# Optimization experiments

Measured on AMD Instinct MI355X. Metric: run time of the kernel, lower is better.

The kernel has to match this reference:

```python
import jax, jax.numpy as jnp
import numpy as np

# Standard icosahedron face list (20 faces over 12 vertices).
ICO_FACES = np.array([
    [0, 11, 5], [0, 5, 1], [0, 1, 7], [0, 7, 10], [0, 10, 11],
    [1, 5, 9], [5, 11, 4], [11, 10, 2], [10, 7, 6], [7, 1, 8],
    [3, 9, 4], [3, 4, 2], [3, 2, 6], [3, 6, 8], [3, 8, 9],
    [4, 9, 5], [2, 4, 11], [6, 2, 10], [8, 6, 7], [9, 8, 1],
], dtype=np.int64)


def _ico_face_adjacency():
    # Faces are adjacent iff they share an edge == share exactly 2 vertices.
    adj = np.zeros((20, 20), dtype=np.float32)
    for i in range(20):
        for j in range(i + 1, 20):
            if len(set(ICO_FACES[i]) & set(ICO_FACES[j])) == 2:
                adj[i, j] = adj[j, i] = 1.0
    return jnp.asarray(adj)


def setup_inputs() -> dict:
    key = jax.random.key(0)
    ks = jax.random.split(key, 9)
    B, D = 65536, 512
    def w(k, fan_in, fan_out):
        return jax.random.normal(k, (fan_in, fan_out), jnp.float32) * (1.0 / np.sqrt(fan_in))
    return {
        "z": jax.random.normal(ks[0], (B, D), jnp.float32),
        "W1": w(ks[1], D, 512), "b1": jnp.zeros((512,), jnp.float32),
        "W2": w(ks[2], 512, 256), "b2": jnp.zeros((256,), jnp.float32),
        "W3": w(ks[3], 256, 128), "b3": jnp.zeros((128,), jnp.float32),
        "W4": w(ks[4], 128, 20), "b4": jnp.zeros((20,), jnp.float32),
        "precomputed_adj": _ico_face_adjacency(),  # [20,20], zero diagonal
    }


def reference(z, W1, b1, W2, b2, W3, b3, W4, b4, precomputed_adj):
    # Eval path: dropout = identity, recon_loss = 0.
    h = jax.nn.relu(z @ W1 + b1)
    h = jax.nn.relu(h @ W2 + b2)
    h = jax.nn.relu(h @ W3 + b3)
    face_probs = jax.nn.sigmoid(h @ W4 + b4)          # [B, 20]
    face_mask = (face_probs > 0.5).astype(z.dtype)    # [B, 20]
    # outer(mask, mask) * precomputed adjacency; diagonal of adj is already 0,
    # reproducing the i != j condition of the original triple loop.
    adj_matrix = face_mask[:, :, None] * face_mask[:, None, :] * precomputed_adj  # [B,20,20]
    recon_loss = jnp.asarray(0.0, jnp.float32)
    return (adj_matrix, face_mask, face_probs, recon_loss)
```

## Files before the change

kernel.cpp:

```cpp
#include <hip/hip_runtime.h>
#include <math.h>

#define NT   1024
#define BR   32
#define TAU  1e-3f
#define LIST_CAP 65536

typedef _Float16 half8 __attribute__((ext_vector_type(8)));
typedef float    f32x4 __attribute__((ext_vector_type(4)));

#define SWZ(r) (((r)&7)<<4)

#define PACK_ELS 425984
#define OFF_LIST 16
#define OFF_PH   (16 + LIST_CAP*4)
#define OFF_PL   (OFF_PH + PACK_ELS*2)
#define WS_PACK_NEED (OFF_PL + PACK_ELS*2)
#define WS_F32_NEED  (16 + LIST_CAP*4)

__device__ __forceinline__ int p1(int c){ return ((c&7)<<6)|(c>>3); }
__device__ __forceinline__ int p2(int c){ return ((c&3)<<6)|(c>>2); }
__device__ __forceinline__ int p3(int c){ return ((c&1)<<6)|(c>>1); }

__global__ void pack_w(const float* __restrict__ W1, const float* __restrict__ W2,
                       const float* __restrict__ W3,
                       _Float16* __restrict__ PH, _Float16* __restrict__ PL) {
    int i = blockIdx.x * 256 + threadIdx.x;
    if (i >= PACK_ELS) return;
    const float* W; int N, KS, loc;
    if (i < 262144)            { W = W1; N = 512; KS = 16; loc = i; }
    else if (i < 393216)       { W = W2; N = 256; KS = 16; loc = i - 262144; }
    else                       { W = W3; N = 128; KS = 8;  loc = i - 393216; }
    int j   = loc & 7;
    int l   = (loc >> 3) & 63;
    int rest = loc >> 9;
    int ks  = rest & (KS - 1);
    int nt  = rest >> (KS == 16 ? 4 : 3);
    int k = ks * 32 + (l >> 4) * 8 + j;
    int n = nt * 16 + (l & 15);
    float v = W[k * N + n];
    _Float16 hi = (_Float16)v;
    _Float16 lo = (_Float16)(v - (float)hi);
    PH[i] = hi; PL[i] = lo;
}

template<int K, int N, int NTW, int MREP, bool SPLIT_OUT>
__device__ __forceinline__ void mfma_layer(const char* __restrict__ actIn,
    const _Float16* __restrict__ PH, const _Float16* __restrict__ PL,
    const float* __restrict__ bias,
    char* __restrict__ actOut, float* __restrict__ h3out,
    int nt0, int m0, int l)
{
    constexpr int KS = K / 32;
    const int r  = l & 15;
    const int kg = l >> 4;
    f32x4 acc[MREP][NTW];
#pragma unroll
    for (int t = 0; t < NTW; ++t) {
        float bb = bias[(nt0 + t) * 16 + r];
#pragma unroll
        for (int m = 0; m < MREP; ++m) acc[m][t] = (f32x4){bb, bb, bb, bb};
    }
    constexpr int loIn = BR * K * 2;
    for (int ks = 0; ks < KS; ++ks) {
        half8 ah[MREP], al[MREP];
#pragma unroll
        for (int m = 0; m < MREP; ++m) {
            int row = (m0 + m) * 16 + r;
            int lin = (row * K + kg * 8 + ks * 32) * 2;
            int sw  = lin ^ SWZ(row);
            ah[m] = *(const half8*)(actIn + sw);
            al[m] = *(const half8*)(actIn + sw + loIn);
        }
#pragma unroll
        for (int t = 0; t < NTW; ++t) {
            const size_t base = ((size_t)((nt0 + t) * KS + ks) * 64 + l) * 8;
            half8 bh = *(const half8*)(PH + base);
            half8 bl = *(const half8*)(PL + base);
#pragma unroll
            for (int m = 0; m < MREP; ++m) {
                acc[m][t] = __builtin_amdgcn_mfma_f32_16x16x32_f16(ah[m], bh, acc[m][t], 0, 0, 0);
                acc[m][t] = __builtin_amdgcn_mfma_f32_16x16x32_f16(ah[m], bl, acc[m][t], 0, 0, 0);
                acc[m][t] = __builtin_amdgcn_mfma_f32_16x16x32_f16(al[m], bh, acc[m][t], 0, 0, 0);
            }
        }
    }
    constexpr int loOut = BR * N * 2;
#pragma unroll
    for (int t = 0; t < NTW; ++t) {
        int n = (nt0 + t) * 16 + r;
#pragma unroll
        for (int m = 0; m < MREP; ++m)
#pragma unroll
        for (int b = 0; b < 4; ++b) {
            int rowD = (m0 + m) * 16 + kg * 4 + b;
            float v = acc[m][t][b];
            v = v > 0.f ? v : 0.f;
            if constexpr (SPLIT_OUT) {
                _Float16 hi = (_Float16)v;
                _Float16 lo = (_Float16)(v - (float)hi);
                int lin = (rowD * N + n) * 2;
                int sw  = lin ^ SWZ(rowD);
                *(_Float16*)(actOut + sw)         = hi;
                *(_Float16*)(actOut + sw + loOut) = lo;
            } else {
                h3out[rowD * 132 + n] = v;
            }
        }
    }
}

__global__ __launch_bounds__(NT, 4)
void dec_mfma(const float* __restrict__ z,
              const float* __restrict__ b1, const float* __restrict__ b2,
              const float* __restrict__ b3,
              const float* __restrict__ W4, const float* __restrict__ b4,
              const float* __restrict__ adj,
              const _Float16* __restrict__ PH, const _Float16* __restrict__ PL,
              float* __restrict__ out, int B,
              int* __restrict__ cnt, int* __restrict__ list)
{
    __shared__ __align__(16) char ldsA[65536];
    __shared__ __align__(16) char ldsB[65536];
    __shared__ float logitsS[BR * 20];
    __shared__ float maskS[BR * 20];
    __shared__ float adjS[400];

    const int tid = threadIdx.x;
    const int w   = tid >> 6;
    const int l   = tid & 63;
    const int rowBase = blockIdx.x * BR;

    const int O_MASK  = B * 400;
    const int O_PROBS = O_MASK + B * 20;
    const int O_LOSS  = O_PROBS + B * 20;

    if (tid < 400) adjS[tid] = adj[tid];

    for (int i = tid; i < BR * 512; i += NT) {
        int r = i >> 9, k = i & 511;
        float v = z[(rowBase + r) * 512 + k];
        _Float16 hi = (_Float16)v;
        _Float16 lo = (_Float16)(v - (float)hi);
        int lin = (r * 512 + k) * 2;
        int sw  = lin ^ SWZ(r);
        *(_Float16*)(ldsA + sw)         = hi;
        *(_Float16*)(ldsA + sw + 32768) = lo;
    }
    __syncthreads();

    mfma_layer<512, 512, 2, 2, true >(ldsA, PH,          PL,          b1, ldsB, nullptr, w * 2, 0, l);
    __syncthreads();
    mfma_layer<512, 256, 1, 2, true >(ldsB, PH + 262144, PL + 262144, b2, ldsA, nullptr, w, 0, l);
    __syncthreads();
    mfma_layer<256, 128, 1, 1, false>(ldsA, PH + 393216, PL + 393216, b3, nullptr, (float*)ldsB, w & 7, w >> 3, l);
    __syncthreads();

    const float* h3 = (const float*)ldsB;
    for (int o = tid; o < BR * 20; o += NT) {
        int r = o / 20, c = o - r * 20;
        float acc = b4[c];
        for (int k = 0; k < 128; ++k)
            acc += h3[r * 132 + k] * W4[k * 20 + c];
        logitsS[o] = acc;
    }
    __syncthreads();

    if (tid < BR) {
        float mn = 1e30f;
#pragma unroll
        for (int c = 0; c < 20; ++c)
            mn = fminf(mn, fabsf(logitsS[tid * 20 + c]));
        if (mn < TAU) {
            int idx = atomicAdd(cnt, 1);
            if (idx < LIST_CAP) list[idx] = rowBase + tid;
        }
    }

    for (int o = tid; o < BR * 20; o += NT) {
        double lg = (double)logitsS[o];
        double p  = 1.0 / (1.0 + exp(-lg));
        out[O_PROBS + rowBase * 20 + o] = (float)p;
        float m = lg > 0.0 ? 1.0f : 0.0f;
        out[O_MASK + rowBase * 20 + o] = m;
        maskS[o] = m;
    }
    __syncthreads();

    for (int o = tid; o < BR * 20; o += NT) {
        int r = o / 20, ii = o - r * 20;
        float mri = maskS[r * 20 + ii];
        float* orow = &out[(rowBase + r) * 400 + ii * 20];
#pragma unroll
        for (int b = 0; b < 5; ++b) {
            float4 v;
            v.x = mri * maskS[r * 20 + 4*b+0] * adjS[ii * 20 + 4*b+0];
            v.y = mri * maskS[r * 20 + 4*b+1] * adjS[ii * 20 + 4*b+1];
            v.z = mri * maskS[r * 20 + 4*b+2] * adjS[ii * 20 + 4*b+2];
            v.w = mri * maskS[r * 20 + 4*b+3] * adjS[ii * 20 + 4*b+3];
            *(float4*)&orow[4*b] = v;
        }
    }

    if (blockIdx.x == 0 && tid == 0) out[O_LOSS] = 0.0f;
}

template<typename T, bool FLAG>
__global__ __launch_bounds__(256, 2)
void dec_fused(const float* __restrict__ z,
               const float* __restrict__ W1, const float* __restrict__ b1,
               const float* __restrict__ W2, const float* __restrict__ b2,
               const float* __restrict__ W3, const float* __restrict__ b3,
               const float* __restrict__ W4, const float* __restrict__ b4,
               const float* __restrict__ adj,
               float* __restrict__ out, int B,
               int* __restrict__ cnt, int* __restrict__ list)
{
    constexpr int STR = (sizeof(T) == 4) ? 20 : 17;
    __shared__ T     hT[512 * STR];
    __shared__ T     logitsS[16 * 20];
    __shared__ float maskS[16 * 20];
    __shared__ float adjS[400];

    const int tid = threadIdx.x;
    const int rg  = tid >> 6;
    const int cg  = tid & 63;
    const int r0  = rg * 4;
    const int rowBase = blockIdx.x * 16;

    const int O_MASK  = B * 400;
    const int O_PROBS = O_MASK + B * 20;
    const int O_LOSS  = O_PROBS + B * 20;

    for (int i = tid; i < 400; i += 256) adjS[i] = adj[i];
    for (int i = tid; i < 512 * 16; i += 256) {
        int k = i & 511, r = i >> 9;
        hT[k * STR + r] = (T)z[(rowBase + r) * 512 + k];
    }
    __syncthreads();
    {
        T a[4][8];
#pragma unroll
        for (int ri = 0; ri < 4; ++ri)
#pragma unroll
            for (int ci = 0; ci < 8; ++ci) a[ri][ci] = (T)0;
#pragma unroll 2
        for (int k = 0; k < 512; ++k) {
            T zr[4];
#pragma unroll
            for (int ri = 0; ri < 4; ++ri) zr[ri] = hT[k * STR + r0 + ri];
            const float4* w1p = (const float4*)(W1 + k * 512 + cg * 8);
            float4 w0 = w1p[0], w1v = w1p[1];
            T wv[8] = {(T)w0.x,(T)w0.y,(T)w0.z,(T)w0.w,
                       (T)w1v.x,(T)w1v.y,(T)w1v.z,(T)w1v.w};
#pragma unroll
            for (int ci = 0; ci < 8; ++ci)
#pragma unroll
                for (int ri = 0; ri < 4; ++ri)
                    a[ri][ci] += zr[ri] * wv[ci];
        }
        __syncthreads();
#pragma unroll
        for (int ci = 0; ci < 8; ++ci) {
            int c = cg * 8 + ci;
            T bb = (T)b1[c]; int cp = p1(c);
#pragma unroll
            for (int ri = 0; ri < 4; ++ri) {
                T v = a[ri][ci] + bb;
                hT[cp * STR + r0 + ri] = v > (T)0 ? v : (T)0;
            }
        }
        __syncthreads();
    }
    {
        T a[4][4];
#pragma unroll
        for (int ri = 0; ri < 4; ++ri)
#pragma unroll
            for (int ci = 0; ci < 4; ++ci) a[ri][ci] = (T)0;
#pragma unroll 2
        for (int k = 0; k < 512; ++k) {
            int kp = p1(k);
            T zr[4];
#pragma unroll
            for (int ri = 0; ri < 4; ++ri) zr[ri] = hT[kp * STR + r0 + ri];
            float4 wq = *(const float4*)(W2 + k * 256 + cg * 4);
            T wv[4] = {(T)wq.x,(T)wq.y,(T)wq.z,(T)wq.w};
#pragma unroll
            for (int ci = 0; ci < 4; ++ci)
#pragma unroll
                for (int ri = 0; ri < 4; ++ri)
                    a[ri][ci] += zr[ri] * wv[ci];
        }
        __syncthreads();
#pragma unroll
        for (int ci = 0; ci < 4; ++ci) {
            int c = cg * 4 + ci;
            T bb = (T)b2[c]; int cp = p2(c);
#pragma unroll
            for (int ri = 0; ri < 4; ++ri) {
                T v = a[ri][ci] + bb;
                hT[cp * STR + r0 + ri] = v > (T)0 ? v : (T)0;
            }
        }
        __syncthreads();
    }
    {
        T a[4][2];
#pragma unroll
        for (int ri = 0; ri < 4; ++ri)
#pragma unroll
            for (int ci = 0; ci < 2; ++ci) a[ri][ci] = (T)0;
#pragma unroll 2
        for (int k = 0; k < 256; ++k) {
            int kp = p2(k);
            T zr[4];
#pragma unroll
            for (int ri = 0; ri < 4; ++ri) zr[ri] = hT[kp * STR + r0 + ri];
            float2 wq = *(const float2*)(W3 + k * 128 + cg * 2);
            T wv[2] = {(T)wq.x,(T)wq.y};
#pragma unroll
            for (int ci = 0; ci < 2; ++ci)
#pragma unroll
                for (int ri = 0; ri < 4; ++ri)
                    a[ri][ci] += zr[ri] * wv[ci];
        }
        __syncthreads();
#pragma unroll
        for (int ci = 0; ci < 2; ++ci) {
            int c = cg * 2 + ci;
            T bb = (T)b3[c]; int cp = p3(c);
#pragma unroll
            for (int ri = 0; ri < 4; ++ri) {
                T v = a[ri][ci] + bb;
                hT[cp * STR + r0 + ri] = v > (T)0 ? v : (T)0;
            }
        }
        __syncthreads();
    }
    for (int o = tid; o < 16 * 20; o += 256) {
        int r = o / 20, c = o - r * 20;
        T acc = (T)b4[c];
        for (int k = 0; k < 128; ++k)
            acc += hT[p3(k) * STR + r] * (T)W4[k * 20 + c];
        logitsS[o] = acc;
    }
    __syncthreads();
    if constexpr (FLAG) {
        if (tid < 16) {
            float mn = 1e30f;
#pragma unroll
            for (int c = 0; c < 20; ++c)
                mn = fminf(mn, fabsf((float)logitsS[tid * 20 + c]));
            if (mn < TAU) {
                int idx = atomicAdd(cnt, 1);
                if (idx < LIST_CAP) list[idx] = rowBase + tid;
            }
        }
    }
    for (int o = tid; o < 16 * 20; o += 256) {
        double lg = (double)logitsS[o];
        double p  = 1.0 / (1.0 + exp(-lg));
        out[O_PROBS + rowBase * 20 + o] = (float)p;
        float m = lg > 0.0 ? 1.0f : 0.0f;
        out[O_MASK + rowBase * 20 + o] = m;
        maskS[o] = m;
    }
    __syncthreads();
    for (int o = tid; o < 16 * 20; o += 256) {
        int r = o / 20, ii = o - r * 20;
        float mri = maskS[r * 20 + ii];
        float* orow = &out[(rowBase + r) * 400 + ii * 20];
#pragma unroll
        for (int b = 0; b < 5; ++b) {
            float4 v;
            v.x = mri * maskS[r * 20 + 4*b+0] * adjS[ii * 20 + 4*b+0];
            v.y = mri * maskS[r * 20 + 4*b+1] * adjS[ii * 20 + 4*b+1];
            v.z = mri * maskS[r * 20 + 4*b+2] * adjS[ii * 20 + 4*b+2];
            v.w = mri * maskS[r * 20 + 4*b+3] * adjS[ii * 20 + 4*b+3];
            *(float4*)&orow[4*b] = v;
        }
    }
    if (blockIdx.x == 0 && tid == 0) out[O_LOSS] = 0.0f;
}

__global__ __launch_bounds__(256, 4)
void repair_rows(const float* __restrict__ z,
                 const float* __restrict__ W1, const float* __restrict__ b1,
                 const float* __restrict__ W2, const float* __restrict__ b2,
                 const float* __restrict__ W3, const float* __restrict__ b3,
                 const float* __restrict__ W4, const float* __restrict__ b4,
                 const float* __restrict__ adj,
                 float* __restrict__ out, int B,
                 const int* __restrict__ cnt, const int* __restrict__ list)
{
    __shared__ double bufA[512];
    __shared__ double bufB[512];
    __shared__ double lgS[20];
    __shared__ float  mskS[20];

    const int tid = threadIdx.x;
    const int O_MASK  = B * 400;
    const int O_PROBS = O_MASK + B * 20;

    int n = *cnt;
    if (n > LIST_CAP) n = LIST_CAP;

    for (int i = blockIdx.x; i < n; i += gridDim.x) {
        int row = list[i];
        for (int k = tid; k < 512; k += 256)
            bufA[k] = (double)z[(size_t)row * 512 + k];
        __syncthreads();
        {
            int c0 = tid, c1 = tid + 256;
            double a0 = (double)b1[c0], a1 = (double)b1[c1];
            for (int k = 0; k < 512; ++k) {
                double h = bufA[k];
                a0 += h * (double)W1[k * 512 + c0];
                a1 += h * (double)W1[k * 512 + c1];
            }
            __syncthreads();
            bufB[c0] = a0 > 0.0 ? a0 : 0.0;
            bufB[c1] = a1 > 0.0 ? a1 : 0.0;
            __syncthreads();
        }
        {
            double a0 = (double)b2[tid < 256 ? tid : 0];
            if (tid < 256)
                for (int k = 0; k < 512; ++k)
                    a0 += bufB[k] * (double)W2[k * 256 + tid];
            __syncthreads();
            if (tid < 256) bufA[tid] = a0 > 0.0 ? a0 : 0.0;
            __syncthreads();
        }
        {
            double a0 = (double)b3[tid < 128 ? tid : 0];
            if (tid < 128)
                for (int k = 0; k < 256; ++k)
                    a0 += bufA[k] * (double)W3[k * 128 + tid];
            __syncthreads();
            if (tid < 128) bufB[tid] = a0 > 0.0 ? a0 : 0.0;
            __syncthreads();
        }
        if (tid < 20) {
            double a0 = (double)b4[tid];
            for (int k = 0; k < 128; ++k)
                a0 += bufB[k] * (double)W4[k * 20 + tid];
            lgS[tid] = a0;
        }
        __syncthreads();
        if (tid < 20) {
            double lg = lgS[tid];
            out[O_PROBS + (size_t)row * 20 + tid] = (float)(1.0 / (1.0 + exp(-lg)));
            float m = lg > 0.0 ? 1.0f : 0.0f;
            out[O_MASK + (size_t)row * 20 + tid] = m;
            mskS[tid] = m;
        }
        __syncthreads();
        for (int o = tid; o < 400; o += 256) {
            int ii = o / 20, jj = o - ii * 20;
            out[(size_t)row * 400 + o] = mskS[ii] * mskS[jj] * adj[o];
        }
        __syncthreads();
    }
}

extern "C" void kernel_launch(void* const* d_in, const int* in_sizes, int n_in,
                              void* d_out, int out_size, void* d_ws, size_t ws_size,
                              hipStream_t stream) {
    const float* z   = (const float*)d_in[0];
    const float* W1  = (const float*)d_in[1];
    const float* b1  = (const float*)d_in[2];
    const float* W2  = (const float*)d_in[3];
    const float* b2  = (const float*)d_in[4];
    const float* W3  = (const float*)d_in[5];
    const float* b3  = (const float*)d_in[6];
    const float* W4  = (const float*)d_in[7];
    const float* b4  = (const float*)d_in[8];
    const float* adj = (const float*)d_in[9];
    float* out = (float*)d_out;

    const int B = in_sizes[0] / 512;

    if (ws_size >= (size_t)WS_PACK_NEED) {
        int* cnt  = (int*)d_ws;
        int* list = (int*)((char*)d_ws + OFF_LIST);
        _Float16* PH = (_Float16*)((char*)d_ws + OFF_PH);
        _Float16* PL = (_Float16*)((char*)d_ws + OFF_PL);
        hipMemsetAsync(d_ws, 0, 16, stream);
        hipLaunchKernelGGL(pack_w, dim3((PACK_ELS + 255) / 256), dim3(256), 0, stream,
                           W1, W2, W3, PH, PL);
        hipLaunchKernelGGL(dec_mfma, dim3(B / BR), dim3(NT), 0, stream,
                           z, b1, b2, b3, W4, b4, adj, PH, PL, out, B, cnt, list);
        hipLaunchKernelGGL(repair_rows, dim3(1024), dim3(256), 0, stream,
                           z, W1, b1, W2, b2, W3, b3, W4, b4, adj, out, B, cnt, list);
    } else if (ws_size >= (size_t)WS_F32_NEED) {
        int* cnt  = (int*)d_ws;
        int* list = (int*)((char*)d_ws + OFF_LIST);
        hipMemsetAsync(d_ws, 0, 16, stream);
        hipLaunchKernelGGL((dec_fused<float, true>), dim3(B / 16), dim3(256), 0, stream,
                           z, W1, b1, W2, b2, W3, b3, W4, b4, adj, out, B, cnt, list);
        hipLaunchKernelGGL(repair_rows, dim3(1024), dim3(256), 0, stream,
                           z, W1, b1, W2, b2, W3, b3, W4, b4, adj, out, B, cnt, list);
    } else {
        hipLaunchKernelGGL((dec_fused<double, false>), dim3(B / 16), dim3(256), 0, stream,
                           z, W1, b1, W2, b2, W3, b3, W4, b4, adj, out, B,
                           (int*)nullptr, (int*)nullptr);
    }
}
```

Measured before the change: 474.5 us.

## Software-pipeline MFMA operand loads and vectorize z staging into LDS

Restructures the MFMA inner loop so weight fragments are prefetched two K-steps ahead from global memory and activation fragments one step ahead from LDS, using register rotation, so memory latency overlaps the MFMA chain. It also replaces the scalar z load and split loop with per-thread float4 loads of 16 contiguous values and 16-byte half8 LDS stores. The prefetch depth raises VGPR pressure at 1024 threads per block, which could cause spills or lower occupancy.

Result: faster. 455.6 us (-4.0%).

```diff
diff --git a/kernel.cpp b/kernel.cpp
--- a/kernel.cpp
+++ b/kernel.cpp
@@ -62,29 +62,64 @@
         for (int m = 0; m < MREP; ++m) acc[m][t] = (f32x4){bb, bb, bb, bb};
     }
     constexpr int loIn = BR * K * 2;
+
+#define AADDR(m, ks) ((((((m0 + (m)) * 16 + r) * K + kg * 8 + (ks) * 32) * 2) ^ SWZ((m0 + (m)) * 16 + r)))
+#define BIDX(t, ks)  (((size_t)((nt0 + (t)) * KS + (ks)) * 64 + l) * 8)
+
+    half8 ah0[MREP], al0[MREP];
+    half8 bh0[NTW],  bl0[NTW];
+    half8 bh1[NTW],  bl1[NTW];
+#pragma unroll
+    for (int m = 0; m < MREP; ++m) {
+        int ao = AADDR(m, 0);
+        ah0[m] = *(const half8*)(actIn + ao);
+        al0[m] = *(const half8*)(actIn + ao + loIn);
+    }
+#pragma unroll
+    for (int t = 0; t < NTW; ++t) {
+        bh0[t] = *(const half8*)(PH + BIDX(t, 0));
+        bl0[t] = *(const half8*)(PL + BIDX(t, 0));
+        bh1[t] = *(const half8*)(PH + BIDX(t, 1));
+        bl1[t] = *(const half8*)(PL + BIDX(t, 1));
+    }
+
+#pragma unroll
     for (int ks = 0; ks < KS; ++ks) {
-        half8 ah[MREP], al[MREP];
-#pragma unroll
-        for (int m = 0; m < MREP; ++m) {
-            int row = (m0 + m) * 16 + r;
-            int lin = (row * K + kg * 8 + ks * 32) * 2;
-            int sw  = lin ^ SWZ(row);
-            ah[m] = *(const half8*)(actIn + sw);
-            al[m] = *(const half8*)(actIn + sw + loIn);
-        }
+        half8 bh2[NTW], bl2[NTW], ahn[MREP], aln[MREP];
+        if (ks + 2 < KS) {
+#pragma unroll
+            for (int t = 0; t < NTW; ++t) {
+                bh2[t] = *(const half8*)(PH + BIDX(t, ks + 2));
+                bl2[t] = *(const half8*)(PL + BIDX(t, ks + 2));
+            }
+        }
+        if (ks + 1 < KS) {
+#pragma unroll
+            for (int m = 0; m < MREP; ++m) {
+                int ao = AADDR(m, ks + 1);
+                ahn[m] = *(const half8*)(actIn + ao);
+                aln[m] = *(const half8*)(actIn + ao + loIn);
+            }
+        }
+#pragma unroll
+        for (int t = 0; t < NTW; ++t)
+#pragma unroll
+            for (int m = 0; m < MREP; ++m) {
+                acc[m][t] = __builtin_amdgcn_mfma_f32_16x16x32_f16(ah0[m], bh0[t], acc[m][t], 0, 0, 0);
+                acc[m][t] = __builtin_amdgcn_mfma_f32_16x16x32_f16(ah0[m], bl0[t], acc[m][t], 0, 0, 0);
+                acc[m][t] = __builtin_amdgcn_mfma_f32_16x16x32_f16(al0[m], bh0[t], acc[m][t], 0, 0, 0);
+            }
 #pragma unroll
         for (int t = 0; t < NTW; ++t) {
-            const size_t base = ((size_t)((nt0 + t) * KS + ks) * 64 + l) * 8;
-            half8 bh = *(const half8*)(PH + base);
-            half8 bl = *(const half8*)(PL + base);
-#pragma unroll
-            for (int m = 0; m < MREP; ++m) {
-                acc[m][t] = __builtin_amdgcn_mfma_f32_16x16x32_f16(ah[m], bh, acc[m][t], 0, 0, 0);
-                acc[m][t] = __builtin_amdgcn_mfma_f32_16x16x32_f16(ah[m], bl, acc[m][t], 0, 0, 0);
-                acc[m][t] = __builtin_amdgcn_mfma_f32_16x16x32_f16(al[m], bh, acc[m][t], 0, 0, 0);
-            }
-        }
-    }
+            bh0[t] = bh1[t]; bl0[t] = bl1[t];
+            bh1[t] = bh2[t]; bl1[t] = bl2[t];
+        }
+#pragma unroll
+        for (int m = 0; m < MREP; ++m) { ah0[m] = ahn[m]; al0[m] = aln[m]; }
+    }
+#undef AADDR
+#undef BIDX
+
     constexpr int loOut = BR * N * 2;
 #pragma unroll
     for (int t = 0; t < NTW; ++t) {
@@ -137,15 +172,30 @@
 
     if (tid < 400) adjS[tid] = adj[tid];
 
-    for (int i = tid; i < BR * 512; i += NT) {
-        int r = i >> 9, k = i & 511;
-        float v = z[(rowBase + r) * 512 + k];
-        _Float16 hi = (_Float16)v;
-        _Float16 lo = (_Float16)(v - (float)hi);
-        int lin = (r * 512 + k) * 2;
-        int sw  = lin ^ SWZ(r);
-        *(_Float16*)(ldsA + sw)         = hi;
-        *(_Float16*)(ldsA + sw + 32768) = lo;
+    {
+        int r   = tid >> 5;
+        int c16 = (tid & 31) * 16;
+        const float4* zp = (const float4*)(z + (size_t)(rowBase + r) * 512 + c16);
+        float4 f0 = zp[0], f1 = zp[1], f2 = zp[2], f3 = zp[3];
+        float fv[16] = {f0.x,f0.y,f0.z,f0.w, f1.x,f1.y,f1.z,f1.w,
+                        f2.x,f2.y,f2.z,f2.w, f3.x,f3.y,f3.z,f3.w};
+        half8 hi0, hi1, lo0, lo1;
+#pragma unroll
+        for (int j = 0; j < 8; ++j) {
+            _Float16 h = (_Float16)fv[j];
+            hi0[j] = h; lo0[j] = (_Float16)(fv[j] - (float)h);
+        }
+#pragma unroll
+        for (int j = 0; j < 8; ++j) {
+            _Float16 h = (_Float16)fv[8 + j];
+            hi1[j] = h; lo1[j] = (_Float16)(fv[8 + j] - (float)h);
+        }
+        int lin = (r * 512 + c16) * 2;
+        int swz = SWZ(r);
+        *(half8*)(ldsA + ((lin     ) ^ swz))          = hi0;
+        *(half8*)(ldsA + ((lin + 16) ^ swz))          = hi1;
+        *(half8*)(ldsA + ((lin     ) ^ swz) + 32768)  = lo0;
+        *(half8*)(ldsA + ((lin + 16) ^ swz) + 32768)  = lo1;
     }
     __syncthreads();
 
```
